# Optimization experiments

Hardware: AMD Instinct MI355X
Metric: run time of the kernel (lower is better)

Reference implementation:

```python
import jax, jax.numpy as jnp
import numpy as np

HIDDEN = 2048
N_HEADS = 32
HEAD_DIM = HIDDEN // N_HEADS  # 64
SEQ = 2048
BATCH = 1
CHUNK = 256
TOPK = 4
THETA = 10000.0
EPS = 1e-6
NEG = jnp.float32(-1e30)


def setup_inputs() -> dict:
    key = jax.random.key(0)
    ks = jax.random.split(key, 8)
    s = 0.02
    return {
        "hidden_states": jax.random.normal(ks[0], (BATCH, SEQ, HIDDEN), jnp.float32),
        "Wq": jax.random.normal(ks[1], (HIDDEN, HIDDEN), jnp.float32) * s,
        "Wk": jax.random.normal(ks[2], (HIDDEN, HIDDEN), jnp.float32) * s,
        "Wv": jax.random.normal(ks[3], (HIDDEN, HIDDEN), jnp.float32) * s,
        "Wo": jax.random.normal(ks[4], (HIDDEN, HIDDEN), jnp.float32) * s,
        "Wg1": jax.random.normal(ks[5], (HEAD_DIM, HIDDEN), jnp.float32) * s,
        "Wg2": jax.random.normal(ks[6], (HIDDEN, HEAD_DIM), jnp.float32) * s,
        "o_norm_weight": jnp.ones((HEAD_DIM,), jnp.float32),
    }


def _rope(t):
    # t: [B, S, H, D]; non-interleaved (NeoX-style) rotary over full head dim
    D = t.shape[-1]
    pos = jnp.arange(t.shape[1], dtype=jnp.float32)
    inv_freq = 1.0 / (THETA ** (jnp.arange(0, D, 2, dtype=jnp.float32) / D))
    freqs = pos[:, None] * inv_freq[None, :]            # [S, D/2]
    cos = jnp.cos(freqs)[None, :, None, :]
    sin = jnp.sin(freqs)[None, :, None, :]
    t1, t2 = t[..., : D // 2], t[..., D // 2:]
    return jnp.concatenate([t1 * cos - t2 * sin, t1 * sin + t2 * cos], axis=-1)


def reference(hidden_states, Wq, Wk, Wv, Wo, Wg1, Wg2, o_norm_weight):
    B, S, _ = hidden_states.shape
    H, D, C = N_HEADS, HEAD_DIM, CHUNK
    NC = S // C

    q = (hidden_states @ Wq.T).reshape(B, S, H, D)
    k = (hidden_states @ Wk.T).reshape(B, S, H, D)
    v = (hidden_states @ Wv.T).reshape(B, S, H, D)
    q, k = _rope(q), _rope(k)

    # --- MoBA gating: per-chunk mean-pooled keys scored against each query ---
    kmean = k.reshape(B, NC, C, H, D).mean(axis=2)           # [B, NC, H, D]
    gate = jnp.einsum('bshd,bnhd->bhsn', q, kmean)           # [B, H, S, NC]

    pos = jnp.arange(S)
    q_chunk = pos // C                                       # [S]
    chunk_ids = jnp.arange(NC)
    future = chunk_ids[None, :] > q_chunk[:, None]           # [S, NC]
    self_blk = chunk_ids[None, :] == q_chunk[:, None]
    gate = jnp.where(future[None, None], NEG, gate)
    gate = jnp.where(self_blk[None, None], -NEG, gate)       # self block always selected

    _, topk_idx = jax.lax.top_k(gate, TOPK)                  # [B, H, S, TOPK]
    sel = jax.nn.one_hot(topk_idx, NC, dtype=jnp.bool_).any(axis=-2)  # [B, H, S, NC]

    # --- block-sparse causal attention over selected chunks ---
    allowed = jnp.take(sel, q_chunk, axis=-1)                # [B, H, S, S] key j -> chunk j//C
    causal = pos[None, :] <= pos[:, None]                    # [S, S]
    allowed = allowed & causal[None, None]

    scale = 1.0 / np.sqrt(D)
    scores = jnp.einsum('bshd,bthd->bhst', q, k) * scale
    scores = jnp.where(allowed, scores, NEG)
    p = jax.nn.softmax(scores, axis=-1)
    o = jnp.einsum('bhst,bthd->bshd', p, v)                  # [B, S, H, D]

    # --- gated RMSNorm (FusedRMSNormGated, sigmoid activation) ---
    g = ((hidden_states @ Wg1.T) @ Wg2.T).reshape(B, S, H, D)
    rms = jax.lax.rsqrt(jnp.mean(o * o, axis=-1, keepdims=True) + EPS)
    o = o * rms * o_norm_weight * jax.nn.sigmoid(g)

    return (o.reshape(B, S, H * D)) @ Wo.T
```

## Files before the change

### kernel.cpp

```cpp
#include <hip/hip_runtime.h>
#include <hip/hip_bf16.h>


typedef __attribute__((ext_vector_type(8))) short s8v;
typedef __attribute__((ext_vector_type(4))) float f4v;

#define MFMA16(A,B,C) __builtin_amdgcn_mfma_f32_16x16x32_bf16(A,B,C,0,0,0)

__device__ __forceinline__ unsigned short f2b_rne(float f){
  unsigned u = __builtin_bit_cast(unsigned, f);
  u = (u + 0x7FFFu + ((u>>16)&1u)) >> 16;
  return (unsigned short)u;
}
__device__ __forceinline__ float b2f(unsigned short h){
  unsigned u = ((unsigned)h)<<16;
  return __builtin_bit_cast(float, u);
}
__device__ __forceinline__ unsigned pack2(float a, float b){
  return (unsigned)f2b_rne(a) | ((unsigned)f2b_rne(b)<<16);
}
__device__ __forceinline__ void gld16(const void* g, void* l){
  __builtin_amdgcn_global_load_lds((const __attribute__((address_space(1))) void*)g,
                                   (__attribute__((address_space(3))) void*)l, 16, 0, 0);
}

__global__ __launch_bounds__(256) void rtab_k(double2* __restrict__ tab){
  const int i = blockIdx.x*256 + threadIdx.x;
  if (i >= 2048*32) return;
  const int d2 = i & 31, s = i >> 5;
  const double invf = 1.0 / pow(10000.0, (double)d2 / 32.0);
  const double ph = (double)s * invf;
  tab[i] = make_double2(cos(ph), sin(ph));
}

__global__ __launch_bounds__(256) void f2b4_k(const float* __restrict__ s,
                                              unsigned short* __restrict__ d, int n4){
  int i = blockIdx.x*256 + threadIdx.x;
  if (i >= n4) return;
  const float4 v = *(const float4*)(s + (size_t)i*4);
  uint2 p; p.x = pack2(v.x, v.y); p.y = pack2(v.z, v.w);
  *(uint2*)(d + (size_t)i*4) = p;
}

__global__ __launch_bounds__(256) void f2bs_k(const float* __restrict__ s,
    unsigned short* __restrict__ hi, unsigned short* __restrict__ lo, int n4){
  int i = blockIdx.x*256 + threadIdx.x;
  if (i >= n4) return;
  const float4 v = *(const float4*)(s + (size_t)i*4);
  unsigned short h0 = f2b_rne(v.x), h1 = f2b_rne(v.y), h2 = f2b_rne(v.z), h3 = f2b_rne(v.w);
  uint2 ph; ph.x = (unsigned)h0 | ((unsigned)h1<<16); ph.y = (unsigned)h2 | ((unsigned)h3<<16);
  uint2 pl; pl.x = pack2(v.x - b2f(h0), v.y - b2f(h1));
  pl.y = pack2(v.z - b2f(h2), v.w - b2f(h3));
  *(uint2*)(hi + (size_t)i*4) = ph;
  *(uint2*)(lo + (size_t)i*4) = pl;
}

__global__ __launch_bounds__(1024) void wsum_k(const float* __restrict__ hs,
    const double2* __restrict__ tab, double* __restrict__ Ac, double* __restrict__ As){
  const int n = blockIdx.x, d2 = blockIdx.y, tid = threadIdx.x;
  double ac0=0, as0=0, ac1=0, as1=0;
  for (int i = 0; i < 256; ++i) {
    const int s = n*256 + i;
    const double2 t = tab[s*32 + d2];
    const double v0 = (double)hs[(size_t)s*2048 + tid];
    const double v1 = (double)hs[(size_t)s*2048 + tid + 1024];
    ac0 += t.x*v0; as0 += t.y*v0;
    ac1 += t.x*v1; as1 += t.y*v1;
  }
  const size_t ro = (size_t)(n*32 + d2)*2048;
  Ac[ro + tid]      = ac0*(1.0/256.0);
  Ac[ro + tid+1024] = ac1*(1.0/256.0);
  As[ro + tid]      = as0*(1.0/256.0);
  As[ro + tid+1024] = as1*(1.0/256.0);
}

__global__ __launch_bounds__(256) void transd_k(const double* __restrict__ in,
    double* __restrict__ out, int R, int C){
  __shared__ double t[64][65];
  const int c0 = blockIdx.x*64, r0 = blockIdx.y*64;
  const int tx = threadIdx.x & 63, ty4 = threadIdx.x >> 6;
  #pragma unroll
  for (int rr = 0; rr < 16; ++rr) {
    const int r = ty4*16 + rr;
    t[r][tx] = in[(size_t)(r0+r)*C + c0+tx];
  }
  __syncthreads();
  #pragma unroll
  for (int rr = 0; rr < 16; ++rr) {
    const int c = ty4*16 + rr;
    out[(size_t)(c0+c)*R + r0+tx] = t[tx][c];
  }
}

__global__ __launch_bounds__(256) void transf_k(const float* __restrict__ in,
    float* __restrict__ out, int R, int C){
  __shared__ float t[64][65];
  const int c0 = blockIdx.x*64, r0 = blockIdx.y*64;
  const int tx = threadIdx.x & 63, ty4 = threadIdx.x >> 6;
  #pragma unroll
  for (int rr = 0; rr < 16; ++rr) {
    const int r = ty4*16 + rr;
    t[r][tx] = in[(size_t)(r0+r)*C + c0+tx];
  }
  __syncthreads();
  #pragma unroll
  for (int rr = 0; rr < 16; ++rr) {
    const int c = ty4*16 + rr;
    out[(size_t)(c0+c)*R + r0+tx] = t[tx][c];
  }
}

__global__ __launch_bounds__(1024) void kmean2_k(const double* __restrict__ AcT,
    const double* __restrict__ AsT, const float* __restrict__ WkT,
    double* __restrict__ Km){
  const int n = blockIdx.x, h = blockIdx.y;
  const int tid = threadIdx.x, d = tid & 63, p = tid >> 6;
  const int d2 = d & 31;
  const bool hiHalf = d >= 32;
  double a = 0.0, b = 0.0;
  #pragma unroll 4
  for (int c = p*128; c < p*128 + 128; ++c) {
    const double x  = AcT[(size_t)c*256 + n*32 + d2];
    const double y  = AsT[(size_t)c*256 + n*32 + d2];
    const double w1 = (double)WkT[(size_t)c*2048 + h*64 + d2];
    const double w2 = (double)WkT[(size_t)c*2048 + h*64 + d2 + 32];
    if (!hiHalf) { a += x*w1; b += y*w2; }
    else         { a += y*w1; b += x*w2; }
  }
  __shared__ double red[1024];
  red[tid] = hiHalf ? (a + b) : (a - b);
  __syncthreads();
  if (p < 8) red[tid] += red[tid + 512];
  __syncthreads();
  if (p < 4) red[tid] += red[tid + 256];
  __syncthreads();
  if (p < 2) red[tid] += red[tid + 128];
  __syncthreads();
  if (p == 0)
    Km[(size_t)(n*32 + h)*64 + d] = red[d] + red[d + 64];
}

__global__ __launch_bounds__(256) void gate_topk_k(const float* __restrict__ Qf,
    const double* __restrict__ Km, unsigned char* __restrict__ Allow,
    unsigned char* __restrict__ Flags){
  const int h = blockIdx.x, c = blockIdx.y, t = threadIdx.x;
  __shared__ double km[512];
  km[t]     = Km[((t>>6)*32 + h)*64 + (t&63)];
  km[t+256] = Km[(((t+256)>>6)*32 + h)*64 + (t&63)];
  __syncthreads();
  const int s = c*256 + t;
  const float* qp = Qf + (size_t)s*2048 + h*64;
  double g[8] = {};
  for (int d = 0; d < 64; ++d) {
    const double qv = (double)qp[d];
    #pragma unroll
    for (int n2 = 0; n2 < 8; ++n2) g[n2] += qv*km[n2*64+d];
  }
  double margin = 1e300;
  if (c >= 4) {
    unsigned pm = 0;
    double v[4];
    for (int rep = 0; rep < 4; ++rep) {
      double best = -1e308; int bi = 0;
      #pragma unroll
      for (int n2 = 0; n2 < 8; ++n2) {
        const bool take = (n2 < c) && !((pm>>n2)&1u) && (g[n2] > best);
        best = take ? g[n2] : best;
        bi   = take ? n2 : bi;
      }
      v[rep] = best; pm |= 1u<<bi;
    }
    margin = v[2] - v[3];
  }
  Flags[h*2048 + s] = (margin < 1e-3) ? 1 : 0;
  #pragma unroll
  for (int n2 = 0; n2 < 8; ++n2) if (n2 > c) g[n2] = -1e300;
  g[c] = 1e300;
  unsigned mask = 0;
  for (int rep = 0; rep < 4; ++rep) {
    double best = -1e308; int bi = 0;
    #pragma unroll
    for (int n2 = 0; n2 < 8; ++n2) {
      const bool take = !((mask>>n2)&1u) && (g[n2] > best);
      best = take ? g[n2] : best;
      bi   = take ? n2 : bi;
    }
    mask |= 1u<<bi;
  }
  Allow[h*2048 + s] = (unsigned char)mask;
}

__global__ __launch_bounds__(64) void repair_k(
    const float* __restrict__ hs, const float* __restrict__ Wq,
    const double2* __restrict__ tab, const double* __restrict__ Km,
    const unsigned char* __restrict__ Flags, unsigned char* __restrict__ Allow)
{
  const int s = blockIdx.x, d = threadIdx.x;
  __shared__ double qr[64];
  __shared__ double g8[8];
  for (int h = 0; h < 32; ++h) {
    if (!Flags[h*2048 + s]) continue;
    const float* hrow = hs + (size_t)s*2048;
    const float* wrow = Wq + (size_t)(h*64 + d)*2048;
    double a0=0,a1=0,a2=0,a3=0;
    for (int k = 0; k < 2048; k += 4) {
      a0 += (double)hrow[k]  *(double)wrow[k];
      a1 += (double)hrow[k+1]*(double)wrow[k+1];
      a2 += (double)hrow[k+2]*(double)wrow[k+2];
      a3 += (double)hrow[k+3]*(double)wrow[k+3];
    }
    qr[d] = (a0+a1)+(a2+a3);
    __syncthreads();
    const double2 t = tab[s*32 + (d&31)];
    const double rot = (d < 32) ? (qr[d]*t.x - qr[d+32]*t.y)
                                : (qr[d-32]*t.y + qr[d]*t.x);
    __syncthreads();
    qr[d] = rot;
    __syncthreads();
    if (d < 8) {
      double g = 0;
      const double* kmp = Km + (size_t)(d*32 + h)*64;
      for (int dd = 0; dd < 64; ++dd) g += qr[dd]*kmp[dd];
      g8[d] = g;
    }
    __syncthreads();
    if (d == 0) {
      const int c = s >> 8;
      double g[8];
      #pragma unroll
      for (int n2 = 0; n2 < 8; ++n2)
        g[n2] = (n2 > c) ? -1e300 : ((n2 == c) ? 1e300 : g8[n2]);
      unsigned mask = 0;
      for (int rep = 0; rep < 4; ++rep) {
        double best = -1e308; int bi = 0;
        #pragma unroll
        for (int n2 = 0; n2 < 8; ++n2) {
          const bool take = !((mask>>n2)&1u) && (g[n2] > best);
          best = take ? g[n2] : best;
          bi   = take ? n2 : bi;
        }
        mask |= 1u<<bi;
      }
      Allow[h*2048 + s] = (unsigned char)mask;
    }
    __syncthreads();
  }
}

__global__ __launch_bounds__(256) void gemm4_bt(
    const unsigned short* __restrict__ Ah, const unsigned short* __restrict__ Al,
    const unsigned short* __restrict__ Bh, const unsigned short* __restrict__ Bl,
    float* __restrict__ C, int M, int N, int K)
{
  alignas(16) __shared__ char SAh[16384];
  alignas(16) __shared__ char SAl[16384];
  alignas(16) __shared__ char SBh[16384];
  alignas(16) __shared__ char SBl[16384];
  const int t = threadIdx.x;
  const int wave = t>>6, lane = t&63, lg = lane>>4, lr = lane&15;
  const int wm = wave >> 1, wn = wave & 1;
  const int m0 = blockIdx.x*128, n0 = blockIdx.y*128;
  const unsigned short* Ahb = Ah + (size_t)m0*K;
  const unsigned short* Alb = Al + (size_t)m0*K;
  const unsigned short* Bhb = Bh + (size_t)n0*K;
  const unsigned short* Blb = Bl + (size_t)n0*K;
  f4v acc[4][4] = {};
  #pragma unroll 1
  for (int kt = 0; kt < K; kt += 64) {
    __syncthreads();
    #pragma unroll
    for (int i = 0; i < 4; ++i) {
      const size_t go = (size_t)(i*32 + (t>>3))*K + kt + (t&7)*8;
      gld16(Ahb + go, SAh + i*4096 + wave*1024);
      gld16(Alb + go, SAl + i*4096 + wave*1024);
      gld16(Bhb + go, SBh + i*4096 + wave*1024);
      gld16(Blb + go, SBl + i*4096 + wave*1024);
    }
    __syncthreads();
    #pragma unroll
    for (int kk = 0; kk < 2; ++kk) {
      s8v ah[4], al[4], bh[4], bl[4];
      #pragma unroll
      for (int i = 0; i < 4; ++i) {
        const int ro = (wm*64 + i*16 + lr)*128 + kk*64 + lg*16;
        ah[i] = *(const s8v*)&SAh[ro];
        al[i] = *(const s8v*)&SAl[ro];
      }
      #pragma unroll
      for (int j = 0; j < 4; ++j) {
        const int ro = (wn*64 + j*16 + lr)*128 + kk*64 + lg*16;
        bh[j] = *(const s8v*)&SBh[ro];
        bl[j] = *(const s8v*)&SBl[ro];
      }
      #pragma unroll
      for (int i = 0; i < 4; ++i)
        #pragma unroll
        for (int j = 0; j < 4; ++j) {
          f4v a = acc[i][j];
          a = MFMA16(ah[i], bh[j], a);
          a = MFMA16(ah[i], bl[j], a);
          a = MFMA16(al[i], bh[j], a);
          a = MFMA16(al[i], bl[j], a);
          acc[i][j] = a;
        }
    }
  }
  #pragma unroll
  for (int i = 0; i < 4; ++i)
    #pragma unroll
    for (int j = 0; j < 4; ++j) {
      const int row = m0 + wm*64 + i*16 + lg*4;
      const int col = n0 + wn*64 + j*16 + lr;
      #pragma unroll
      for (int r = 0; r < 4; ++r)
        C[(size_t)(row+r)*N + col] = acc[i][j][r];
    }
}

template<int BM, int BN, int WN, bool OUTBF>
__global__ __launch_bounds__(256) void gemm_bt(
    const unsigned short* __restrict__ A, const unsigned short* __restrict__ B,
    void* __restrict__ C, int M, int N, int K)
{
  alignas(16) __shared__ char AsB[BM*128];
  alignas(16) __shared__ char BsB[BN*128];
  const int t = threadIdx.x;
  const int wave = t>>6, lane = t&63, lg = lane>>4, lr = lane&15;
  const int wm = wave / WN, wn = wave % WN;
  const int m0 = blockIdx.x*BM, n0 = blockIdx.y*BN;
  const unsigned short* Ab = A + (size_t)m0*K;
  const unsigned short* Bb = B + (size_t)n0*K;
  f4v acc[4][4] = {};
  #pragma unroll 1
  for (int kt = 0; kt < K; kt += 64) {
    __syncthreads();
    #pragma unroll
    for (int i = 0; i < BM/32; ++i)
      gld16(Ab + (size_t)(i*32 + (t>>3))*K + kt + (t&7)*8, AsB + i*4096 + wave*1024);
    #pragma unroll
    for (int i = 0; i < BN/32; ++i)
      gld16(Bb + (size_t)(i*32 + (t>>3))*K + kt + (t&7)*8, BsB + i*4096 + wave*1024);
    __syncthreads();
    #pragma unroll
    for (int kk = 0; kk < 2; ++kk) {
      s8v af[4], bfr[4];
      #pragma unroll
      for (int i = 0; i < 4; ++i)
        af[i] = *(const s8v*)&AsB[(wm*64 + i*16 + lr)*128 + kk*64 + lg*16];
      #pragma unroll
      for (int j = 0; j < 4; ++j)
        bfr[j] = *(const s8v*)&BsB[(wn*64 + j*16 + lr)*128 + kk*64 + lg*16];
      #pragma unroll
      for (int i = 0; i < 4; ++i)
        #pragma unroll
        for (int j = 0; j < 4; ++j)
          acc[i][j] = MFMA16(af[i], bfr[j], acc[i][j]);
    }
  }
  #pragma unroll
  for (int i = 0; i < 4; ++i)
    #pragma unroll
    for (int j = 0; j < 4; ++j) {
      const int row = m0 + wm*64 + i*16 + lg*4;
      const int col = n0 + wn*64 + j*16 + lr;
      #pragma unroll
      for (int r = 0; r < 4; ++r) {
        if (OUTBF) ((unsigned short*)C)[(size_t)(row+r)*N + col] = f2b_rne(acc[i][j][r]);
        else       ((float*)C)[(size_t)(row+r)*N + col] = acc[i][j][r];
      }
    }
}

__global__ __launch_bounds__(256) void rope32q_k(float* __restrict__ Qf,
    unsigned short* __restrict__ Qb, const double2* __restrict__ tab){
  const int idx = blockIdx.x*256 + threadIdx.x;
  const int d2 = idx & 31, hh = (idx>>5)&31, s = idx>>10;
  const double2 t = tab[s*32 + d2];
  const float cs = (float)t.x, sn = (float)t.y;
  const size_t base = (size_t)s*2048 + hh*64 + d2;
  const float q1 = Qf[base], q2 = Qf[base+32];
  const float o1 = q1*cs - q2*sn, o2 = q1*sn + q2*cs;
  Qf[base] = o1; Qf[base+32] = o2;
  Qb[base] = f2b_rne(o1); Qb[base+32] = f2b_rne(o2);
}

__global__ __launch_bounds__(256) void rope32_k(const float* __restrict__ Kf,
    unsigned short* __restrict__ Kb, const double2* __restrict__ tab){
  const int idx = blockIdx.x*256 + threadIdx.x;
  const int d2 = idx & 31, hh = (idx>>5)&31, s = idx>>10;
  const double2 t = tab[s*32 + d2];
  const float cs = (float)t.x, sn = (float)t.y;
  const size_t base = (size_t)s*2048 + hh*64 + d2;
  const float k1 = Kf[base], k2 = Kf[base+32];
  Kb[base]    = f2b_rne(k1*cs - k2*sn);
  Kb[base+32] = f2b_rne(k1*sn + k2*cs);
}

__global__ __launch_bounds__(256) void vtrans_k(const float* __restrict__ V,
                                                unsigned short* __restrict__ Vt){
  __shared__ unsigned short tile[64][68];
  const int s0 = blockIdx.x*64, c0 = blockIdx.y*64;
  const int tx = threadIdx.x & 63, ty = threadIdx.x >> 6;
  #pragma unroll
  for (int rr = 0; rr < 16; ++rr) {
    const int r = ty*16 + rr;
    tile[tx][r] = f2b_rne(V[(size_t)(s0+r)*2048 + c0+tx]);
  }
  __syncthreads();
  #pragma unroll
  for (int rr = 0; rr < 16; ++rr) {
    const int cc = ty*16 + rr;
    Vt[(size_t)(c0+cc)*2048 + s0+tx] = tile[cc][tx];
  }
}

__global__ __launch_bounds__(64) void attn_k(
    const unsigned short* __restrict__ Qb, const unsigned short* __restrict__ Kb,
    const unsigned short* __restrict__ Vt, const float* __restrict__ Gf,
    const unsigned char* __restrict__ Allow, const float* __restrict__ Wn,
    float* __restrict__ Of)
{
  const int h = blockIdx.x, c = blockIdx.y, zb = blockIdx.z;
  const int lane = threadIdx.x, lg = lane>>4, lr = lane&15;
  const int qbase = c*256 + zb*16;
  alignas(16) __shared__ char P[2048];

  const size_t qrow = (size_t)(qbase + lr);
  const s8v qf0 = *(const s8v*)&Qb[qrow*2048 + h*64 + lg*8];
  const s8v qf1 = *(const s8v*)&Qb[qrow*2048 + h*64 + 32 + lg*8];
  const unsigned am = Allow[h*2048 + qrow];
  const int q = qbase + lr;
  const int sw = (lr&7)<<4;

  float mx = -1e30f, ls = 0.f;
  f4v ot[4] = {};

  for (int n = 0; n <= c; ++n) {
    if (!__ballot((am>>n)&1u)) continue;
    const int okc = (am>>n)&1;
    #pragma unroll 1
    for (int t4 = 0; t4 < 4; ++t4) {
      const int kb0 = n*256 + t4*64;
      s8v kf[4][2];
      #pragma unroll
      for (int i = 0; i < 4; ++i) {
        const size_t krow = (size_t)(kb0 + i*16 + lr);
        kf[i][0] = *(const s8v*)&Kb[krow*2048 + h*64 + lg*8];
        kf[i][1] = *(const s8v*)&Kb[krow*2048 + h*64 + 32 + lg*8];
      }
      f4v st[4];
      #pragma unroll
      for (int i = 0; i < 4; ++i) {
        f4v zz = {};
        zz = MFMA16(kf[i][0], qf0, zz);
        st[i] = MFMA16(kf[i][1], qf1, zz);
      }
      float cm = -__builtin_inff();
      #pragma unroll
      for (int i = 0; i < 4; ++i)
        #pragma unroll
        for (int r = 0; r < 4; ++r) {
          float v = st[i][r]*0.125f;
          const int key = kb0 + i*16 + lg*4 + r;
          const bool ok = okc && (n != c || key <= q);
          v = ok ? v : -__builtin_inff();
          st[i][r] = v;
          cm = fmaxf(cm, v);
        }
      cm = fmaxf(cm, __shfl_xor(cm, 16));
      cm = fmaxf(cm, __shfl_xor(cm, 32));
      const float nm = fmaxf(mx, cm);
      const float al = __expf(mx - nm);
      mx = nm;
      float ps = 0.f;
      #pragma unroll
      for (int i = 0; i < 4; ++i) {
        const float p0 = __expf(st[i][0]-mx);
        const float p1 = __expf(st[i][1]-mx);
        const float p2 = __expf(st[i][2]-mx);
        const float p3 = __expf(st[i][3]-mx);
        ps += (p0+p1)+(p2+p3);
        uint2 pk; pk.x = pack2(p0,p1); pk.y = pack2(p2,p3);
        *(uint2*)&P[lr*128 + ((i*32 + lg*8) ^ sw)] = pk;
      }
      ps += __shfl_xor(ps, 16);
      ps += __shfl_xor(ps, 32);
      ls = ls*al + ps;
      #pragma unroll
      for (int jd = 0; jd < 4; ++jd) ot[jd] *= al;
      asm volatile("s_waitcnt lgkmcnt(0)" ::: "memory");
      __builtin_amdgcn_sched_barrier(0);
      #pragma unroll
      for (int kk = 0; kk < 2; ++kk) {
        s8v vfr[4];
        #pragma unroll
        for (int jd = 0; jd < 4; ++jd)
          vfr[jd] = *(const s8v*)&Vt[(size_t)(h*64 + jd*16 + lr)*2048 + kb0 + kk*32 + lg*8];
        const s8v pfr = *(const s8v*)&P[lr*128 + ((kk*64 + lg*16) ^ sw)];
        #pragma unroll
        for (int jd = 0; jd < 4; ++jd)
          ot[jd] = MFMA16(vfr[jd], pfr, ot[jd]);
      }
      asm volatile("s_waitcnt lgkmcnt(0)" ::: "memory");
      __builtin_amdgcn_sched_barrier(0);
    }
  }
  const float inv_ = 1.0f/ls;
  float ssum = 0.f;
  #pragma unroll
  for (int jd = 0; jd < 4; ++jd)
    #pragma unroll
    for (int r = 0; r < 4; ++r) {
      const float o = ot[jd][r]*inv_;
      ot[jd][r] = o;
      ssum += o*o;
    }
  ssum += __shfl_xor(ssum, 16);
  ssum += __shfl_xor(ssum, 32);
  const float rmsv = rsqrtf(ssum*(1.0f/64.0f) + 1e-6f);
  #pragma unroll
  for (int jd = 0; jd < 4; ++jd) {
    const float4 w4 = *(const float4*)&Wn[jd*16 + lg*4];
    const float4 g4 = *(const float4*)&Gf[qrow*2048 + h*64 + jd*16 + lg*4];
    float4 o4;
    o4.x = ot[jd][0]*rmsv*w4.x*(1.0f/(1.0f+__expf(-g4.x)));
    o4.y = ot[jd][1]*rmsv*w4.y*(1.0f/(1.0f+__expf(-g4.y)));
    o4.z = ot[jd][2]*rmsv*w4.z*(1.0f/(1.0f+__expf(-g4.z)));
    o4.w = ot[jd][3]*rmsv*w4.w*(1.0f/(1.0f+__expf(-g4.w)));
    *(float4*)&Of[qrow*2048 + h*64 + jd*16 + lg*4] = o4;
  }
}

extern "C" void kernel_launch(void* const* d_in, const int* in_sizes, int n_in,
                              void* d_out, int out_size, void* d_ws, size_t ws_size,
                              hipStream_t stream)
{
  const float* hs  = (const float*)d_in[0];
  const float* Wq  = (const float*)d_in[1];
  const float* Wk  = (const float*)d_in[2];
  const float* Wv  = (const float*)d_in[3];
  const float* Wo  = (const float*)d_in[4];
  const float* Wg1 = (const float*)d_in[5];
  const float* Wg2 = (const float*)d_in[6];
  const float* Wn  = (const float*)d_in[7];

  const size_t S2 = (size_t)2048*2048;
  const size_t MB = (size_t)1<<20;
  char* ws = (char*)d_ws;
  double2*        tab   = (double2*)       (ws);
  unsigned short* hsh   = (unsigned short*)(ws + 1*MB);
  unsigned short* hsl   = (unsigned short*)(ws + 9*MB);
  unsigned short* Wqh   = (unsigned short*)(ws + 17*MB);
  unsigned short* Wql   = (unsigned short*)(ws + 25*MB);
  unsigned short* Wkb   = (unsigned short*)(ws + 33*MB);
  unsigned short* Wvb   = (unsigned short*)(ws + 41*MB);
  unsigned short* Wg1b  = (unsigned short*)(ws + 49*MB);
  unsigned short* Wg2b  = (unsigned short*)(ws + 49*MB + 262144);
  unsigned short* g1b   = (unsigned short*)(ws + 49*MB + 524288);
  double*         km    = (double*)        (ws + 49*MB + 786432);
  unsigned char*  allow = (unsigned char*) (ws + 49*MB + 917504);
  unsigned char*  flags = (unsigned char*) (ws + 49*MB + 983040);
  float*          qf    = (float*)         (ws + 50*MB);
  float*          kf    = (float*)         (ws + 66*MB);
  float*          vf    = (float*)         (ws + 82*MB);
  double*         Ac    = (double*)        (ws + 98*MB);
  double*         As    = (double*)        (ws + 102*MB);
  unsigned short* kb    = (unsigned short*)(ws + 17*MB);
  unsigned short* qb    = (unsigned short*)(ws + 25*MB);
  double*         AcT   = (double*)        (ws + 33*MB);
  double*         AsT   = (double*)        (ws + 37*MB);
  float*          WkT   = (float*)         (ws + 66*MB);
  unsigned short* vt    = (unsigned short*)(ws + 66*MB);
  unsigned short* ofb   = (unsigned short*)(ws + 74*MB);
  float*          gf    = (float*)         (ws + 82*MB);
  float*          of    = (float*)         (ws + 33*MB);
  unsigned short* Wob   = (unsigned short*)(ws + 50*MB);
  (void)ws_size; (void)in_sizes; (void)n_in; (void)out_size;

  rtab_k<<<256,256,0,stream>>>(tab);
  f2bs_k<<<4096,256,0,stream>>>(hs, hsh, hsl, (int)(S2/4));
  f2bs_k<<<4096,256,0,stream>>>(Wq, Wqh, Wql, (int)(S2/4));
  f2b4_k<<<4096,256,0,stream>>>(Wk, Wkb, (int)(S2/4));
  f2b4_k<<<4096,256,0,stream>>>(Wv, Wvb, (int)(S2/4));
  f2b4_k<<<128,256,0,stream>>>(Wg1, Wg1b, 64*2048/4);
  f2b4_k<<<128,256,0,stream>>>(Wg2, Wg2b, 2048*64/4);

  gemm4_bt<<<dim3(16,16),256,0,stream>>>(hsh, hsl, Wqh, Wql, qf, 2048, 2048, 2048);
  gemm_bt<128,128,2,false><<<dim3(16,16),256,0,stream>>>(hsh, Wkb, kf, 2048, 2048, 2048);
  gemm_bt<128,128,2,false><<<dim3(16,16),256,0,stream>>>(hsh, Wvb, vf, 2048, 2048, 2048);

  rope32q_k<<<8192,256,0,stream>>>(qf, qb, tab);
  rope32_k<<<8192,256,0,stream>>>(kf, kb, tab);

  wsum_k<<<dim3(8,32),1024,0,stream>>>(hs, tab, Ac, As);
  transd_k<<<dim3(32,4),256,0,stream>>>(Ac, AcT, 256, 2048);
  transd_k<<<dim3(32,4),256,0,stream>>>(As, AsT, 256, 2048);
  transf_k<<<dim3(32,32),256,0,stream>>>(Wk, WkT, 2048, 2048);
  kmean2_k<<<dim3(8,32),1024,0,stream>>>(AcT, AsT, WkT, km);
  gate_topk_k<<<dim3(32,8),256,0,stream>>>(qf, km, allow, flags);
  repair_k<<<2048,64,0,stream>>>(hs, Wq, tab, km, flags, allow);

  vtrans_k<<<dim3(32,32),256,0,stream>>>(vf, vt);
  gemm_bt<256,64,1,true><<<dim3(8,1),256,0,stream>>>(hsh, Wg1b, g1b, 2048, 64, 2048);
  gemm_bt<128,128,2,false><<<dim3(16,16),256,0,stream>>>(g1b, Wg2b, gf, 2048, 2048, 64);

  attn_k<<<dim3(32,8,16),64,0,stream>>>(qb, kb, vt, gf, allow, Wn, of);

  f2b4_k<<<4096,256,0,stream>>>(of, ofb, (int)(S2/4));
  f2b4_k<<<4096,256,0,stream>>>(Wo, Wob, (int)(S2/4));
  gemm_bt<128,128,2,false><<<dim3(16,16),256,0,stream>>>(ofb, Wob, d_out, 2048, 2048, 2048);
}
```

Before: 752.9 us.

## Fuse wsum transposes, shuffle P in registers, emit bf16 attention output

```diff
diff --git a/kernel.cpp b/kernel.cpp
--- a/kernel.cpp
+++ b/kernel.cpp
@@ -55,40 +55,25 @@
   *(uint2*)(lo + (size_t)i*4) = pl;
 }
 
-__global__ __launch_bounds__(1024) void wsum_k(const float* __restrict__ hs,
-    const double2* __restrict__ tab, double* __restrict__ Ac, double* __restrict__ As){
-  const int n = blockIdx.x, d2 = blockIdx.y, tid = threadIdx.x;
-  double ac0=0, as0=0, ac1=0, as1=0;
+__global__ __launch_bounds__(128) void wsum_k(const float* __restrict__ hs,
+    const double2* __restrict__ tab, double* __restrict__ AcT, double* __restrict__ AsT){
+  const int n = blockIdx.x, cq = blockIdx.y;
+  const int c = cq*128 + threadIdx.x;
+  double ac[32] = {}, as_[32] = {};
   for (int i = 0; i < 256; ++i) {
     const int s = n*256 + i;
-    const double2 t = tab[s*32 + d2];
-    const double v0 = (double)hs[(size_t)s*2048 + tid];
-    const double v1 = (double)hs[(size_t)s*2048 + tid + 1024];
-    ac0 += t.x*v0; as0 += t.y*v0;
-    ac1 += t.x*v1; as1 += t.y*v1;
-  }
-  const size_t ro = (size_t)(n*32 + d2)*2048;
-  Ac[ro + tid]      = ac0*(1.0/256.0);
-  Ac[ro + tid+1024] = ac1*(1.0/256.0);
-  As[ro + tid]      = as0*(1.0/256.0);
-  As[ro + tid+1024] = as1*(1.0/256.0);
-}
-
-__global__ __launch_bounds__(256) void transd_k(const double* __restrict__ in,
-    double* __restrict__ out, int R, int C){
-  __shared__ double t[64][65];
-  const int c0 = blockIdx.x*64, r0 = blockIdx.y*64;
-  const int tx = threadIdx.x & 63, ty4 = threadIdx.x >> 6;
-  #pragma unroll
-  for (int rr = 0; rr < 16; ++rr) {
-    const int r = ty4*16 + rr;
-    t[r][tx] = in[(size_t)(r0+r)*C + c0+tx];
-  }
-  __syncthreads();
-  #pragma unroll
-  for (int rr = 0; rr < 16; ++rr) {
-    const int c = ty4*16 + rr;
-    out[(size_t)(c0+c)*R + r0+tx] = t[tx][c];
+    const double v = (double)hs[(size_t)s*2048 + c];
+    #pragma unroll
+    for (int d2 = 0; d2 < 32; ++d2) {
+      const double2 t = tab[s*32 + d2];
+      ac[d2]  += t.x*v;
+      as_[d2] += t.y*v;
+    }
+  }
+  #pragma unroll
+  for (int d2 = 0; d2 < 32; ++d2) {
+    AcT[(size_t)c*256 + n*32 + d2] = ac[d2]*(1.0/256.0);
+    AsT[(size_t)c*256 + n*32 + d2] = as_[d2]*(1.0/256.0);
   }
 }
 
@@ -414,23 +399,22 @@
   }
 }
 
-__global__ __launch_bounds__(64) void attn_k(
+__global__ __launch_bounds__(256) void attn_k(
     const unsigned short* __restrict__ Qb, const unsigned short* __restrict__ Kb,
     const unsigned short* __restrict__ Vt, const float* __restrict__ Gf,
     const unsigned char* __restrict__ Allow, const float* __restrict__ Wn,
-    float* __restrict__ Of)
+    unsigned short* __restrict__ Ob)
 {
-  const int h = blockIdx.x, c = blockIdx.y, zb = blockIdx.z;
-  const int lane = threadIdx.x, lg = lane>>4, lr = lane&15;
-  const int qbase = c*256 + zb*16;
-  alignas(16) __shared__ char P[2048];
-
+  const int h = blockIdx.x, c = blockIdx.y;
+  const int t = threadIdx.x, wave = t>>6, lane = t&63, lg = lane>>4, lr = lane&15;
+  const int qbase = c*256 + (blockIdx.z*4 + wave)*16;
   const size_t qrow = (size_t)(qbase + lr);
   const s8v qf0 = *(const s8v*)&Qb[qrow*2048 + h*64 + lg*8];
   const s8v qf1 = *(const s8v*)&Qb[qrow*2048 + h*64 + 32 + lg*8];
   const unsigned am = Allow[h*2048 + qrow];
   const int q = qbase + lr;
-  const int sw = (lr&7)<<4;
+  const int laneA = ((lg&1)<<5) + lr;
+  const bool hiSel = lg >= 2;
 
   float mx = -1e30f, ls = 0.f;
   f4v ot[4] = {};
@@ -472,6 +456,7 @@
       const float nm = fmaxf(mx, cm);
       const float al = __expf(mx - nm);
       mx = nm;
+      uint2 w[4];
       float ps = 0.f;
       #pragma unroll
       for (int i = 0; i < 4; ++i) {
@@ -480,29 +465,38 @@
         const float p2 = __expf(st[i][2]-mx);
         const float p3 = __expf(st[i][3]-mx);
         ps += (p0+p1)+(p2+p3);
-        uint2 pk; pk.x = pack2(p0,p1); pk.y = pack2(p2,p3);
-        *(uint2*)&P[lr*128 + ((i*32 + lg*8) ^ sw)] = pk;
+        w[i].x = pack2(p0,p1);
+        w[i].y = pack2(p2,p3);
       }
       ps += __shfl_xor(ps, 16);
       ps += __shfl_xor(ps, 32);
       ls = ls*al + ps;
       #pragma unroll
       for (int jd = 0; jd < 4; ++jd) ot[jd] *= al;
-      asm volatile("s_waitcnt lgkmcnt(0)" ::: "memory");
-      __builtin_amdgcn_sched_barrier(0);
       #pragma unroll
       for (int kk = 0; kk < 2; ++kk) {
+        const unsigned a0x = __shfl(w[2*kk].x,   laneA);
+        const unsigned a0y = __shfl(w[2*kk].y,   laneA);
+        const unsigned b0x = __shfl(w[2*kk].x,   laneA+16);
+        const unsigned b0y = __shfl(w[2*kk].y,   laneA+16);
+        const unsigned a1x = __shfl(w[2*kk+1].x, laneA);
+        const unsigned a1y = __shfl(w[2*kk+1].y, laneA);
+        const unsigned b1x = __shfl(w[2*kk+1].x, laneA+16);
+        const unsigned b1y = __shfl(w[2*kk+1].y, laneA+16);
+        uint4 uu;
+        uu.x = hiSel ? a1x : a0x;
+        uu.y = hiSel ? a1y : a0y;
+        uu.z = hiSel ? b1x : b0x;
+        uu.w = hiSel ? b1y : b0y;
+        const s8v pfr = __builtin_bit_cast(s8v, uu);
         s8v vfr[4];
         #pragma unroll
         for (int jd = 0; jd < 4; ++jd)
           vfr[jd] = *(const s8v*)&Vt[(size_t)(h*64 + jd*16 + lr)*2048 + kb0 + kk*32 + lg*8];
-        const s8v pfr = *(const s8v*)&P[lr*128 + ((kk*64 + lg*16) ^ sw)];
         #pragma unroll
         for (int jd = 0; jd < 4; ++jd)
           ot[jd] = MFMA16(vfr[jd], pfr, ot[jd]);
       }
-      asm volatile("s_waitcnt lgkmcnt(0)" ::: "memory");
-      __builtin_amdgcn_sched_barrier(0);
     }
   }
   const float inv_ = 1.0f/ls;
@@ -522,12 +516,12 @@
   for (int jd = 0; jd < 4; ++jd) {
     const float4 w4 = *(const float4*)&Wn[jd*16 + lg*4];
     const float4 g4 = *(const float4*)&Gf[qrow*2048 + h*64 + jd*16 + lg*4];
-    float4 o4;
-    o4.x = ot[jd][0]*rmsv*w4.x*(1.0f/(1.0f+__expf(-g4.x)));
-    o4.y = ot[jd][1]*rmsv*w4.y*(1.0f/(1.0f+__expf(-g4.y)));
-    o4.z = ot[jd][2]*rmsv*w4.z*(1.0f/(1.0f+__expf(-g4.z)));
-    o4.w = ot[jd][3]*rmsv*w4.w*(1.0f/(1.0f+__expf(-g4.w)));
-    *(float4*)&Of[qrow*2048 + h*64 + jd*16 + lg*4] = o4;
+    const float o0 = ot[jd][0]*rmsv*w4.x*(1.0f/(1.0f+__expf(-g4.x)));
+    const float o1 = ot[jd][1]*rmsv*w4.y*(1.0f/(1.0f+__expf(-g4.y)));
+    const float o2 = ot[jd][2]*rmsv*w4.z*(1.0f/(1.0f+__expf(-g4.z)));
+    const float o3 = ot[jd][3]*rmsv*w4.w*(1.0f/(1.0f+__expf(-g4.w)));
+    uint2 pk; pk.x = pack2(o0,o1); pk.y = pack2(o2,o3);
+    *(uint2*)&Ob[qrow*2048 + h*64 + jd*16 + lg*4] = pk;
   }
 }
 
@@ -563,17 +557,14 @@
   float*          qf    = (float*)         (ws + 50*MB);
   float*          kf    = (float*)         (ws + 66*MB);
   float*          vf    = (float*)         (ws + 82*MB);
-  double*         Ac    = (double*)        (ws + 98*MB);
-  double*         As    = (double*)        (ws + 102*MB);
   unsigned short* kb    = (unsigned short*)(ws + 17*MB);
   unsigned short* qb    = (unsigned short*)(ws + 25*MB);
   double*         AcT   = (double*)        (ws + 33*MB);
   double*         AsT   = (double*)        (ws + 37*MB);
   float*          WkT   = (float*)         (ws + 66*MB);
   unsigned short* vt    = (unsigned short*)(ws + 66*MB);
-  unsigned short* ofb   = (unsigned short*)(ws + 74*MB);
+  unsigned short* ob    = (unsigned short*)(ws + 74*MB);
   float*          gf    = (float*)         (ws + 82*MB);
-  float*          of    = (float*)         (ws + 33*MB);
   unsigned short* Wob   = (unsigned short*)(ws + 50*MB);
   (void)ws_size; (void)in_sizes; (void)n_in; (void)out_size;
 
@@ -592,9 +583,7 @@
   rope32q_k<<<8192,256,0,stream>>>(qf, qb, tab);
   rope32_k<<<8192,256,0,stream>>>(kf, kb, tab);
 
-  wsum_k<<<dim3(8,32),1024,0,stream>>>(hs, tab, Ac, As);
-  transd_k<<<dim3(32,4),256,0,stream>>>(Ac, AcT, 256, 2048);
-  transd_k<<<dim3(32,4),256,0,stream>>>(As, AsT, 256, 2048);
+  wsum_k<<<dim3(8,16),128,0,stream>>>(hs, tab, AcT, AsT);
   transf_k<<<dim3(32,32),256,0,stream>>>(Wk, WkT, 2048, 2048);
   kmean2_k<<<dim3(8,32),1024,0,stream>>>(AcT, AsT, WkT, km);
   gate_topk_k<<<dim3(32,8),256,0,stream>>>(qf, km, allow, flags);
@@ -604,9 +593,8 @@
   gemm_bt<256,64,1,true><<<dim3(8,1),256,0,stream>>>(hsh, Wg1b, g1b, 2048, 64, 2048);
   gemm_bt<128,128,2,false><<<dim3(16,16),256,0,stream>>>(g1b, Wg2b, gf, 2048, 2048, 64);
 
-  attn_k<<<dim3(32,8,16),64,0,stream>>>(qb, kb, vt, gf, allow, Wn, of);
-
-  f2b4_k<<<4096,256,0,stream>>>(of, ofb, (int)(S2/4));
+  attn_k<<<dim3(32,8,4),256,0,stream>>>(qb, kb, vt, gf, allow, Wn, ob);
+
   f2b4_k<<<4096,256,0,stream>>>(Wo, Wob, (int)(S2/4));
-  gemm_bt<128,128,2,false><<<dim3(16,16),256,0,stream>>>(ofb, Wob, d_out, 2048, 2048, 2048);
-}
+  gemm_bt<128,128,2,false><<<dim3(16,16),256,0,stream>>>(ob, Wob, d_out, 2048, 2048, 2048);
+}
```

Result: slower. 828.3 us (+10.0%).
